# Kernel optimization log

Hardware: AMD Instinct MI355X
Metric: run time of the kernel (lower is better)

The kernel has to match this reference:

```python
import jax, jax.numpy as jnp
import numpy as np

B, S, E, H, L = 4, 1024, 1024, 16, 4
D = E // H
MAX_POS = 1024
NI, NS = 10000, 1000
W_SCALE = 0.02


def setup_inputs() -> dict:
    key = jax.random.key(0)
    ks = jax.random.split(key, 24)
    r = lambda k, sh: jax.random.normal(k, sh, dtype=jnp.float32) * W_SCALE
    return {
        'item_inputs': jax.random.randint(ks[0], (B, S), 0, NI),
        'skill_inputs': jax.random.randint(ks[1], (B, S), 0, NS),
        'label_inputs': jax.random.randint(ks[2], (B, S), 0, 2),
        'item_ids': jax.random.randint(ks[3], (B, S), 0, NI),
        'skill_ids': jax.random.randint(ks[4], (B, S), 0, NS),
        'emb_item': r(ks[5], (NI, E)),
        'emb_skill': r(ks[6], (NS, E)),
        'W_in': r(ks[7], (E, 2 * E)),
        'b_in': r(ks[8], (E,)),
        'Wq': r(ks[9], (L, E, E)),
        'bq': r(ks[10], (L, E)),
        'Wk': r(ks[11], (L, E, E)),
        'bk': r(ks[12], (L, E)),
        'Wv': r(ks[13], (L, E, E)),
        'bv': r(ks[14], (L, E)),
        'Wg': r(ks[15], (L, H, E)),
        'bg': r(ks[16], (L, H)),
        'pos_key': r(ks[17], (L, MAX_POS, D)),
        'Wl': r(ks[18], (L, 3, E, E)),
        'bl': r(ks[19], (L, 3, E)),
        'W_out': r(ks[20], (1, E)),
        'b_out': r(ks[21], (1,)),
    }


def _forward(item_inputs, skill_inputs, emb_item, emb_skill, W_in, b_in,
             Wq, bq, Wk, bk, Wv, bv, Wg, bg, pos_key, Wl, bl, W_out, b_out):
    # input embedding: concat(item, skill) -> linear
    x = jnp.concatenate([emb_item[item_inputs], emb_skill[skill_inputs]], axis=-1)
    x = x @ W_in.T + b_in  # [B, S, E]
    pos_ids = jnp.clip(jnp.arange(S), 0, MAX_POS - 1)
    inv_sqrt_d = 1.0 / np.sqrt(D).astype(np.float32)
    for l in range(L):
        # NOTE (faithful to source): k and v are computed from q0 = linear_q(x)
        q0 = x @ Wq[l].T + bq[l]
        k = q0 @ Wk[l].T + bk[l]
        v = q0 @ Wv[l].T + bv[l]
        # global bias: [B, S, H] -> [B, H, S, 1] (broadcast over key dim)
        glo = jnp.transpose(k @ Wg[l].T + bg[l], (0, 2, 1))[..., None]
        qh = q0.reshape(B, S, H, D).transpose(0, 2, 1, 3)  # [B,H,S,D]
        kh = k.reshape(B, S, H, D).transpose(0, 2, 1, 3)
        vh = v.reshape(B, S, H, D).transpose(0, 2, 1, 3)
        pe = pos_key[l][pos_ids]  # [S, D]
        scores = (jnp.einsum('bhqd,bhkd->bhqk', qh, kh)
                  + glo
                  + jnp.einsum('bhqd,kd->bhqk', qh, pe)) * inv_sqrt_d
        prob = jax.nn.softmax(scores, axis=-1)
        o = jnp.einsum('bhqk,bhkd->bhqd', prob, vh)
        o = o.transpose(0, 2, 1, 3).reshape(B, S, E)
        for i in range(3):  # GELU MLP stack
            o = jax.nn.gelu(o @ Wl[l, i].T + bl[l, i], approximate=False)
        x = o
    out = x @ W_out.T + b_out  # [B, S, 1]
    return out[..., 0]


def reference(item_inputs, skill_inputs, label_inputs, item_ids, skill_ids,
              emb_item, emb_skill, W_in, b_in, Wq, bq, Wk, bk, Wv, bv,
              Wg, bg, pos_key, Wl, bl, W_out, b_out):
    return _forward(item_inputs, skill_inputs, emb_item, emb_skill, W_in, b_in,
                    Wq, bq, Wk, bk, Wv, bv, Wg, bg, pos_key, Wl, bl, W_out, b_out)
```

## Files before the change

kernel.cpp:

```cpp
#include <hip/hip_runtime.h>
#include <hip/hip_bf16.h>


#define B_ 4
#define S_ 1024
#define E_ 1024
#define H_ 16
#define D_ 64
#define L_ 4
#define M_ (B_ * S_)
#define EE (E_ * E_)

typedef __attribute__((ext_vector_type(8))) __bf16 bf16x8;
typedef __attribute__((ext_vector_type(4))) __bf16 bf16x4;
typedef __attribute__((ext_vector_type(4))) float f32x4;
typedef __attribute__((ext_vector_type(8))) unsigned short u16x8;

__device__ __forceinline__ float bf2f(unsigned short u) {
    union { unsigned int i; float f; } x;
    x.i = ((unsigned int)u) << 16;
    return x.f;
}
__device__ __forceinline__ float gelu_exact(float x) {
    return 0.5f * x * (1.0f + erff(x * 0.70710678118654752f));
}

__device__ __forceinline__ size_t kpack_idx(int m, int col) {
    const int b = m >> 10, srow = m & (S_ - 1);
    const int h = col >> 6, d = col & 63;
    const int bh = b * H_ + h;
    const int kt = srow >> 6, kb = (srow >> 4) & 3, l15 = srow & 15;
    const int kc = d >> 5, lhi = (d >> 3) & 3, j = d & 7;
    const int frag = ((bh * 16 + kt) * 4 + kb) * 2 + kc;
    return (size_t)frag * 512 + (size_t)(lhi * 16 + l15) * 8 + j;
}
__device__ __forceinline__ size_t vpack_idx(int m, int col) {
    const int b = m >> 10, key = m & (S_ - 1);
    const int h = col >> 6, d = col & 63;
    const int bh = b * H_ + h;
    const int kt = key >> 6;
    const int k6 = key & 63;
    const int kc = k6 >> 5, kl = k6 & 31;
    const int lhi = (kl >> 2) & 3;
    const int j = ((kl >> 4) << 2) | (kl & 3);
    const int db = d >> 4, l15 = d & 15;
    const int frag = ((bh * 16 + kt) * 4 + db) * 2 + kc;
    return (size_t)frag * 512 + (size_t)(lhi * 16 + l15) * 8 + j;
}

__global__ __launch_bounds__(256) void cvt_f32_bf16(
    const float* __restrict__ in, __bf16* __restrict__ out, int n) {
    const int i = (blockIdx.x * 256 + threadIdx.x) * 4;
    if (i >= n) return;
    const float4 v = *(const float4*)(in + i);
    __bf16* o = out + i;
    o[0] = (__bf16)v.x; o[1] = (__bf16)v.y; o[2] = (__bf16)v.z; o[3] = (__bf16)v.w;
}

__global__ __launch_bounds__(256) void cvt_layer_weights(
    const float* __restrict__ Wq, const float* __restrict__ Wk,
    const float* __restrict__ Wv, const float* __restrict__ Wl,
    __bf16* __restrict__ out) {
    const int i = (blockIdx.x * 256 + threadIdx.x) * 4;
    const int mat = i >> 20;
    const int off = i & (EE - 1);
    const float* src = (mat == 0) ? Wq : (mat == 1) ? Wk : (mat == 2) ? Wv
                                        : Wl + (size_t)(mat - 3) * EE;
    const float4 v = *(const float4*)(src + off);
    __bf16* o = out + i;
    o[0] = (__bf16)v.x; o[1] = (__bf16)v.y; o[2] = (__bf16)v.z; o[3] = (__bf16)v.w;
}

__global__ __launch_bounds__(256) void embed_gather(
    const int* __restrict__ item_idx, const int* __restrict__ skill_idx,
    const float* __restrict__ emb_item, const float* __restrict__ emb_skill,
    __bf16* __restrict__ Xc) {
    const int r = blockIdx.x;
    const int c = threadIdx.x * 8;
    const float* s = (c < E_) ? emb_item + (size_t)item_idx[r] * E_ + c
                              : emb_skill + (size_t)skill_idx[r] * E_ + (c - E_);
    const float4 a = *(const float4*)s;
    const float4 b = *(const float4*)(s + 4);
    __bf16* o = Xc + (size_t)r * 2048 + c;
    o[0] = (__bf16)a.x; o[1] = (__bf16)a.y; o[2] = (__bf16)a.z; o[3] = (__bf16)a.w;
    o[4] = (__bf16)b.x; o[5] = (__bf16)b.y; o[6] = (__bf16)b.z; o[7] = (__bf16)b.w;
}

template <int ACT, int ADD_PE, int PACK>
__global__ __launch_bounds__(256) void gemm_bf16(
    const __bf16* __restrict__ A, const __bf16* __restrict__ Bm,
    const float* __restrict__ bias, __bf16* __restrict__ C, int K,
    const float* __restrict__ pe, const float* __restrict__ bias2) {
    __shared__ __bf16 As[128 * 64];
    __shared__ __bf16 Bs[64 * 64];
    const int tid = threadIdx.x;
    const int lane = tid & 63;
    const int wid = tid >> 6;
    const int wm = wid >> 1;
    const int wn = wid & 1;
    const int l15 = lane & 15, lhi = lane >> 4;

    const int gx = gridDim.x;
    const int id = blockIdx.y * gx + blockIdx.x;
    const int nwg = gx * gridDim.y;
    const int swz = (id & 7) * (nwg >> 3) + (id >> 3);
    const int m0 = (swz / gx) * 128;
    const int n0 = (swz % gx) * 64;

    const __bf16* pa[4];
    __bf16* la[4];
#pragma unroll
    for (int j = 0; j < 4; ++j) {
        const int ca = wid * 256 + j * 64 + lane;
        const int row = ca >> 3, ch = ca & 7;
        pa[j] = A + (size_t)(m0 + row) * K + ((ch ^ (row & 7)) << 3);
        la[j] = As + (size_t)ca * 8;
    }
    const __bf16* pb[2];
    __bf16* lb[2];
#pragma unroll
    for (int j = 0; j < 2; ++j) {
        const int cb = wid * 128 + j * 64 + lane;
        const int row = cb >> 3, ch = cb & 7;
        pb[j] = Bm + (size_t)(n0 + row) * K + ((ch ^ (row & 7)) << 3);
        lb[j] = Bs + (size_t)cb * 8;
    }

    int aoff[4][2], boff[2][2];
#pragma unroll
    for (int mi = 0; mi < 4; ++mi) {
        const int row = wm * 64 + mi * 16 + l15;
#pragma unroll
        for (int kc = 0; kc < 2; ++kc)
            aoff[mi][kc] = row * 64 + (((kc * 4 + lhi) ^ (row & 7)) << 3);
    }
#pragma unroll
    for (int ni = 0; ni < 2; ++ni) {
        const int row = wn * 32 + ni * 16 + l15;
#pragma unroll
        for (int kc = 0; kc < 2; ++kc)
            boff[ni][kc] = row * 64 + (((kc * 4 + lhi) ^ (row & 7)) << 3);
    }

    f32x4 acc[4][2] = {};

    for (int k0 = 0; k0 < K; k0 += 64) {
#pragma unroll
        for (int j = 0; j < 4; ++j)
            __builtin_amdgcn_global_load_lds(
                (const __attribute__((address_space(1))) unsigned int*)(pa[j] + k0),
                (__attribute__((address_space(3))) unsigned int*)la[j], 16, 0, 0);
#pragma unroll
        for (int j = 0; j < 2; ++j)
            __builtin_amdgcn_global_load_lds(
                (const __attribute__((address_space(1))) unsigned int*)(pb[j] + k0),
                (__attribute__((address_space(3))) unsigned int*)lb[j], 16, 0, 0);
        __syncthreads();
        bf16x8 af[4][2], bfr[2][2];
#pragma unroll
        for (int mi = 0; mi < 4; ++mi)
#pragma unroll
            for (int kc = 0; kc < 2; ++kc)
                af[mi][kc] = *(const bf16x8*)(As + aoff[mi][kc]);
#pragma unroll
        for (int ni = 0; ni < 2; ++ni)
#pragma unroll
            for (int kc = 0; kc < 2; ++kc)
                bfr[ni][kc] = *(const bf16x8*)(Bs + boff[ni][kc]);
#pragma unroll
        for (int mi = 0; mi < 4; ++mi)
#pragma unroll
            for (int ni = 0; ni < 2; ++ni)
#pragma unroll
                for (int kc = 0; kc < 2; ++kc)
                    acc[mi][ni] = __builtin_amdgcn_mfma_f32_16x16x32_bf16(
                        af[mi][kc], bfr[ni][kc], acc[mi][ni], 0, 0, 0);
        __syncthreads();
    }

    const int ccol0 = n0 + wn * 32 + l15;
    const int crow0 = m0 + wm * 64 + (lhi << 2);
#pragma unroll
    for (int mi = 0; mi < 4; ++mi) {
#pragma unroll
        for (int ni = 0; ni < 2; ++ni) {
            const int col = ccol0 + ni * 16;
            float bsum;
            if (PACK == 3) bsum = (col < 1024) ? bias[col] : bias2[col - 1024];
            else bsum = bias[col];
#pragma unroll
            for (int r = 0; r < 4; ++r) {
                const int row = crow0 + mi * 16 + r;
                float v = acc[mi][ni][r] + bsum;
                if (ADD_PE) v += pe[((row & (S_ - 1)) << 6) + (col & (D_ - 1))];
                if (ACT) v = gelu_exact(v);
                if (PACK == 0) {
                    C[(size_t)row * E_ + col] = (__bf16)v;
                } else if (PACK == 1) {
                    C[kpack_idx(row, col)] = (__bf16)v;
                } else if (PACK == 2) {
                    C[vpack_idx(row, col)] = (__bf16)v;
                } else {
                    if (col < 1024) {
                        v += pe[((row & (S_ - 1)) << 6) + (col & (D_ - 1))];
                        C[kpack_idx(row, col)] = (__bf16)v;
                    } else {
                        C[(size_t)M_ * E_ + vpack_idx(row, col - 1024)] = (__bf16)v;
                    }
                }
            }
        }
    }
}

__global__ __launch_bounds__(512) void attn_mfma(
    const __bf16* __restrict__ Q, const __bf16* __restrict__ Kp,
    const __bf16* __restrict__ Vp, __bf16* __restrict__ O) {
    __shared__ __bf16 Slds[2][2][8 * 512];
    const int tid = threadIdx.x;
    const int lane = tid & 63;
    const int w = tid >> 6;
    const int l15 = lane & 15, lhi = lane >> 4;

    const int id = blockIdx.y * gridDim.x + blockIdx.x;
    const int swz = (id & 7) * 64 + (id >> 3);
    const int q0 = (swz & 7) * 128 + w * 16;
    const int bh = swz >> 3;
    const int bb = bh >> 4, hh = bh & 15;

    bf16x8 qf[2];
    {
        const __bf16* qrow =
            Q + (size_t)(bb * S_ + q0 + l15) * E_ + hh * 64 + lhi * 8;
#pragma unroll
        for (int kc = 0; kc < 2; ++kc) {
            const u16x8 raw = *(const u16x8*)(qrow + kc * 32);
            bf16x8 v;
#pragma unroll
            for (int j = 0; j < 8; ++j) v[j] = (__bf16)(bf2f(raw[j]) * 0.125f);
            qf[kc] = v;
        }
    }

    const __bf16* kpw = Kp + ((size_t)bh * 16 * 8 + w) * 512 + lane * 8;
    const __bf16* vpw = Vp + ((size_t)bh * 16 * 8 + w) * 512 + lane * 8;

    float m_l = -1e30f, l_l = 0.f;
    f32x4 oacc[4] = {};

    __builtin_amdgcn_global_load_lds(
        (const __attribute__((address_space(1))) unsigned int*)(kpw),
        (__attribute__((address_space(3))) unsigned int*)(&Slds[0][0][w * 512]),
        16, 0, 0);
    __builtin_amdgcn_global_load_lds(
        (const __attribute__((address_space(1))) unsigned int*)(vpw),
        (__attribute__((address_space(3))) unsigned int*)(&Slds[0][1][w * 512]),
        16, 0, 0);

#pragma unroll 2
    for (int kt = 0; kt < S_ / 64; ++kt) {
        const int cur = kt & 1;
        __syncthreads();
        if (kt < S_ / 64 - 1) {
            const size_t fo = (size_t)(kt + 1) * 8 * 512;
            __builtin_amdgcn_global_load_lds(
                (const __attribute__((address_space(1))) unsigned int*)(kpw + fo),
                (__attribute__((address_space(3))) unsigned int*)(
                    &Slds[cur ^ 1][0][w * 512]), 16, 0, 0);
            __builtin_amdgcn_global_load_lds(
                (const __attribute__((address_space(1))) unsigned int*)(vpw + fo),
                (__attribute__((address_space(3))) unsigned int*)(
                    &Slds[cur ^ 1][1][w * 512]), 16, 0, 0);
        }
        const __bf16* kl = &Slds[cur][0][0];
        const __bf16* vl = &Slds[cur][1][0];
        f32x4 s[4];
#pragma unroll
        for (int kb = 0; kb < 4; ++kb) {
            const bf16x8 k0 = *(const bf16x8*)(kl + (kb * 2 + 0) * 512 + lane * 8);
            const bf16x8 k1 = *(const bf16x8*)(kl + (kb * 2 + 1) * 512 + lane * 8);
            f32x4 z = {};
            z = __builtin_amdgcn_mfma_f32_16x16x32_bf16(k0, qf[0], z, 0, 0, 0);
            s[kb] = __builtin_amdgcn_mfma_f32_16x16x32_bf16(k1, qf[1], z, 0, 0, 0);
        }
        float mx0 = fmaxf(fmaxf(s[0][0], s[0][1]), fmaxf(s[0][2], s[0][3]));
        float mx1 = fmaxf(fmaxf(s[1][0], s[1][1]), fmaxf(s[1][2], s[1][3]));
        float mx2 = fmaxf(fmaxf(s[2][0], s[2][1]), fmaxf(s[2][2], s[2][3]));
        float mx3 = fmaxf(fmaxf(s[3][0], s[3][1]), fmaxf(s[3][2], s[3][3]));
        float mx = fmaxf(fmaxf(mx0, mx1), fmaxf(mx2, mx3));
        mx = fmaxf(mx, __shfl_xor(mx, 16));
        mx = fmaxf(mx, __shfl_xor(mx, 32));
        const float mnew = fmaxf(m_l, mx);
        const float corr = __expf(m_l - mnew);
        float p[4][4];
        float rs = 0.f;
#pragma unroll
        for (int kb = 0; kb < 4; ++kb) {
            float sb = 0.f;
#pragma unroll
            for (int r = 0; r < 4; ++r) {
                p[kb][r] = __expf(s[kb][r] - mnew);
                sb += p[kb][r];
            }
            rs += sb;
        }
        rs += __shfl_xor(rs, 16);
        rs += __shfl_xor(rs, 32);
        l_l = l_l * corr + rs;
        m_l = mnew;
#pragma unroll
        for (int db = 0; db < 4; ++db)
#pragma unroll
            for (int r = 0; r < 4; ++r) oacc[db][r] *= corr;
        bf16x8 pf[2];
#pragma unroll
        for (int kc = 0; kc < 2; ++kc) {
            bf16x8 v;
#pragma unroll
            for (int r = 0; r < 4; ++r) {
                v[r] = (__bf16)p[kc * 2][r];
                v[r + 4] = (__bf16)p[kc * 2 + 1][r];
            }
            pf[kc] = v;
        }
#pragma unroll
        for (int db = 0; db < 4; ++db) {
            const bf16x8 v0 = *(const bf16x8*)(vl + (db * 2 + 0) * 512 + lane * 8);
            const bf16x8 v1 = *(const bf16x8*)(vl + (db * 2 + 1) * 512 + lane * 8);
            oacc[db] = __builtin_amdgcn_mfma_f32_16x16x32_bf16(v0, pf[0], oacc[db], 0, 0, 0);
            oacc[db] = __builtin_amdgcn_mfma_f32_16x16x32_bf16(v1, pf[1], oacc[db], 0, 0, 0);
        }
    }
    const float inv_l = 1.f / l_l;
    __bf16* orow = O + (size_t)(bb * S_ + q0 + l15) * E_ + hh * 64 + lhi * 4;
#pragma unroll
    for (int db = 0; db < 4; ++db) {
        bf16x4 ov;
#pragma unroll
        for (int r = 0; r < 4; ++r) ov[r] = (__bf16)(oacc[db][r] * inv_l);
        *(bf16x4*)(orow + db * 16) = ov;
    }
}

__global__ __launch_bounds__(256) void final_proj(
    const __bf16* __restrict__ X, const float* __restrict__ Wout,
    const float* __restrict__ bout, float* __restrict__ out) {
    const int wid = threadIdx.x >> 6, lane = threadIdx.x & 63;
    const int m = blockIdx.x * 4 + wid;
    const __bf16* xrow = X + (size_t)m * E_;
    float acc = 0.f;
#pragma unroll
    for (int c = 0; c < 2; ++c) {
        const int idx = c * 512 + lane * 8;
        const u16x8 xv = *(const u16x8*)(xrow + idx);
        const float4 w1 = *(const float4*)(Wout + idx);
        const float4 w2 = *(const float4*)(Wout + idx + 4);
        acc += bf2f(xv[0]) * w1.x + bf2f(xv[1]) * w1.y + bf2f(xv[2]) * w1.z +
               bf2f(xv[3]) * w1.w + bf2f(xv[4]) * w2.x + bf2f(xv[5]) * w2.y +
               bf2f(xv[6]) * w2.z + bf2f(xv[7]) * w2.w;
    }
#pragma unroll
    for (int off = 32; off; off >>= 1) acc += __shfl_xor(acc, off, 64);
    if (lane == 0) out[m] = acc + bout[0];
}

extern "C" void kernel_launch(void* const* d_in, const int* in_sizes, int n_in,
                              void* d_out, int out_size, void* d_ws, size_t ws_size,
                              hipStream_t stream) {
    const int* item_inputs = (const int*)d_in[0];
    const int* skill_inputs = (const int*)d_in[1];
    const float* emb_item = (const float*)d_in[5];
    const float* emb_skill = (const float*)d_in[6];
    const float* W_in = (const float*)d_in[7];
    const float* b_in = (const float*)d_in[8];
    const float* Wq = (const float*)d_in[9];
    const float* bq = (const float*)d_in[10];
    const float* Wk = (const float*)d_in[11];
    const float* bk = (const float*)d_in[12];
    const float* Wv = (const float*)d_in[13];
    const float* bv = (const float*)d_in[14];
    const float* pos_key = (const float*)d_in[17];
    const float* Wl = (const float*)d_in[18];
    const float* bl = (const float*)d_in[19];
    const float* W_out = (const float*)d_in[20];
    const float* b_out = (const float*)d_in[21];
    float* out = (float*)d_out;

    const size_t SZ = (size_t)M_ * E_;
    __bf16* Xc = (__bf16*)d_ws;
    __bf16* X = Xc + (size_t)M_ * 2048;
    __bf16* Qb = X + SZ;
    __bf16* Kp = Qb + SZ;
    __bf16* Vp = Kp + SZ;
    __bf16* Winb = Vp + SZ;
    __bf16* Wbuf = Winb + 2 * EE;

    const dim3 gg(E_ / 64, M_ / 128);
    const dim3 ggkv(2 * E_ / 64, M_ / 128);
    const dim3 bb(256);

    embed_gather<<<dim3(M_), bb, 0, stream>>>(item_inputs, skill_inputs,
                                              emb_item, emb_skill, Xc);
    cvt_f32_bf16<<<dim3(2 * EE / 1024), bb, 0, stream>>>(W_in, Winb, 2 * EE);
    gemm_bf16<0, 0, 0><<<gg, bb, 0, stream>>>(Xc, Winb, b_in, X, 2048, nullptr, nullptr);

    for (int l = 0; l < L_; ++l) {
        cvt_layer_weights<<<dim3(6 * EE / 1024), bb, 0, stream>>>(
            Wq + (size_t)l * EE, Wk + (size_t)l * EE, Wv + (size_t)l * EE,
            Wl + (size_t)l * 3 * EE, Wbuf);
        const float* pe_l = pos_key + (size_t)l * S_ * D_;
        gemm_bf16<0, 0, 0><<<gg, bb, 0, stream>>>(X, Wbuf + 0 * EE, bq + l * E_, Qb, E_, nullptr, nullptr);
        gemm_bf16<0, 0, 3><<<ggkv, bb, 0, stream>>>(Qb, Wbuf + 1 * EE, bk + l * E_, Kp, E_, pe_l, bv + l * E_);
        attn_mfma<<<dim3(S_ / 128, B_ * H_), dim3(512), 0, stream>>>(Qb, Kp, Vp, X);
        gemm_bf16<1, 0, 0><<<gg, bb, 0, stream>>>(X, Wbuf + 3 * EE, bl + (l * 3 + 0) * E_, Qb, E_, nullptr, nullptr);
        gemm_bf16<1, 0, 0><<<gg, bb, 0, stream>>>(Qb, Wbuf + 4 * EE, bl + (l * 3 + 1) * E_, Kp, E_, nullptr, nullptr);
        gemm_bf16<1, 0, 0><<<gg, bb, 0, stream>>>(Kp, Wbuf + 5 * EE, bl + (l * 3 + 2) * E_, X, E_, nullptr, nullptr);
    }
    final_proj<<<dim3(M_ / 4), bb, 0, stream>>>(X, W_out, b_out, out);
}
```

Baseline: 598.5 us.

## Double-buffer GEMM LDS tiles and convert all layer weights in one launch

The GEMM now uses two LDS buffers per operand and issues the async global-to-LDS loads for the next K tile before computing on the current one. This overlaps memory latency with MFMA work and needs one barrier per iteration instead of two. The per-layer weight conversion kernels are merged into a single up-front launch that writes all layers into one larger workspace, removing three launches. The cost is doubled LDS per block, which may reduce occupancy, and a larger workspace requirement.

```diff
diff --git a/kernel.cpp b/kernel.cpp
--- a/kernel.cpp
+++ b/kernel.cpp
@@ -57,15 +57,19 @@
     o[0] = (__bf16)v.x; o[1] = (__bf16)v.y; o[2] = (__bf16)v.z; o[3] = (__bf16)v.w;
 }
 
-__global__ __launch_bounds__(256) void cvt_layer_weights(
+__global__ __launch_bounds__(256) void cvt_all_weights(
     const float* __restrict__ Wq, const float* __restrict__ Wk,
     const float* __restrict__ Wv, const float* __restrict__ Wl,
     __bf16* __restrict__ out) {
     const int i = (blockIdx.x * 256 + threadIdx.x) * 4;
-    const int mat = i >> 20;
-    const int off = i & (EE - 1);
-    const float* src = (mat == 0) ? Wq : (mat == 1) ? Wk : (mat == 2) ? Wv
-                                        : Wl + (size_t)(mat - 3) * EE;
+    const int l = i / (6 * EE);
+    const int r = i - l * 6 * EE;
+    const int mat = r >> 20;
+    const int off = r & (EE - 1);
+    const float* src = (mat == 0) ? Wq + (size_t)l * EE
+                     : (mat == 1) ? Wk + (size_t)l * EE
+                     : (mat == 2) ? Wv + (size_t)l * EE
+                                  : Wl + ((size_t)l * 3 + (mat - 3)) * EE;
     const float4 v = *(const float4*)(src + off);
     __bf16* o = out + i;
     o[0] = (__bf16)v.x; o[1] = (__bf16)v.y; o[2] = (__bf16)v.z; o[3] = (__bf16)v.w;
@@ -91,8 +95,8 @@
     const __bf16* __restrict__ A, const __bf16* __restrict__ Bm,
     const float* __restrict__ bias, __bf16* __restrict__ C, int K,
     const float* __restrict__ pe, const float* __restrict__ bias2) {
-    __shared__ __bf16 As[128 * 64];
-    __shared__ __bf16 Bs[64 * 64];
+    __shared__ __bf16 As[2][128 * 64];
+    __shared__ __bf16 Bs[2][64 * 64];
     const int tid = threadIdx.x;
     const int lane = tid & 63;
     const int wid = tid >> 6;
@@ -108,22 +112,22 @@
     const int n0 = (swz % gx) * 64;
 
     const __bf16* pa[4];
-    __bf16* la[4];
+    int laoff[4];
 #pragma unroll
     for (int j = 0; j < 4; ++j) {
         const int ca = wid * 256 + j * 64 + lane;
         const int row = ca >> 3, ch = ca & 7;
         pa[j] = A + (size_t)(m0 + row) * K + ((ch ^ (row & 7)) << 3);
-        la[j] = As + (size_t)ca * 8;
+        laoff[j] = ca * 8;
     }
     const __bf16* pb[2];
-    __bf16* lb[2];
+    int lboff[2];
 #pragma unroll
     for (int j = 0; j < 2; ++j) {
         const int cb = wid * 128 + j * 64 + lane;
         const int row = cb >> 3, ch = cb & 7;
         pb[j] = Bm + (size_t)(n0 + row) * K + ((ch ^ (row & 7)) << 3);
-        lb[j] = Bs + (size_t)cb * 8;
+        lboff[j] = cb * 8;
     }
 
     int aoff[4][2], boff[2][2];
@@ -143,30 +147,50 @@
     }
 
     f32x4 acc[4][2] = {};
-
-    for (int k0 = 0; k0 < K; k0 += 64) {
-#pragma unroll
-        for (int j = 0; j < 4; ++j)
-            __builtin_amdgcn_global_load_lds(
-                (const __attribute__((address_space(1))) unsigned int*)(pa[j] + k0),
-                (__attribute__((address_space(3))) unsigned int*)la[j], 16, 0, 0);
-#pragma unroll
-        for (int j = 0; j < 2; ++j)
-            __builtin_amdgcn_global_load_lds(
-                (const __attribute__((address_space(1))) unsigned int*)(pb[j] + k0),
-                (__attribute__((address_space(3))) unsigned int*)lb[j], 16, 0, 0);
+    const int NT = K >> 6;
+
+#pragma unroll
+    for (int j = 0; j < 4; ++j)
+        __builtin_amdgcn_global_load_lds(
+            (const __attribute__((address_space(1))) unsigned int*)(pa[j]),
+            (__attribute__((address_space(3))) unsigned int*)(&As[0][0] + laoff[j]),
+            16, 0, 0);
+#pragma unroll
+    for (int j = 0; j < 2; ++j)
+        __builtin_amdgcn_global_load_lds(
+            (const __attribute__((address_space(1))) unsigned int*)(pb[j]),
+            (__attribute__((address_space(3))) unsigned int*)(&Bs[0][0] + lboff[j]),
+            16, 0, 0);
+
+    for (int t = 0; t < NT; ++t) {
+        const int cur = t & 1;
         __syncthreads();
+        if (t + 1 < NT) {
+            const size_t koff = (size_t)(t + 1) << 6;
+#pragma unroll
+            for (int j = 0; j < 4; ++j)
+                __builtin_amdgcn_global_load_lds(
+                    (const __attribute__((address_space(1))) unsigned int*)(pa[j] + koff),
+                    (__attribute__((address_space(3))) unsigned int*)(
+                        &As[cur ^ 1][0] + laoff[j]), 16, 0, 0);
+#pragma unroll
+            for (int j = 0; j < 2; ++j)
+                __builtin_amdgcn_global_load_lds(
+                    (const __attribute__((address_space(1))) unsigned int*)(pb[j] + koff),
+                    (__attribute__((address_space(3))) unsigned int*)(
+                        &Bs[cur ^ 1][0] + lboff[j]), 16, 0, 0);
+        }
         bf16x8 af[4][2], bfr[2][2];
 #pragma unroll
         for (int mi = 0; mi < 4; ++mi)
 #pragma unroll
             for (int kc = 0; kc < 2; ++kc)
-                af[mi][kc] = *(const bf16x8*)(As + aoff[mi][kc]);
+                af[mi][kc] = *(const bf16x8*)(&As[cur][0] + aoff[mi][kc]);
 #pragma unroll
         for (int ni = 0; ni < 2; ++ni)
 #pragma unroll
             for (int kc = 0; kc < 2; ++kc)
-                bfr[ni][kc] = *(const bf16x8*)(Bs + boff[ni][kc]);
+                bfr[ni][kc] = *(const bf16x8*)(&Bs[cur][0] + boff[ni][kc]);
 #pragma unroll
         for (int mi = 0; mi < 4; ++mi)
 #pragma unroll
@@ -175,7 +199,6 @@
                 for (int kc = 0; kc < 2; ++kc)
                     acc[mi][ni] = __builtin_amdgcn_mfma_f32_16x16x32_bf16(
                         af[mi][kc], bfr[ni][kc], acc[mi][ni], 0, 0, 0);
-        __syncthreads();
     }
 
     const int ccol0 = n0 + wn * 32 + l15;
@@ -393,7 +416,7 @@
     __bf16* Kp = Qb + SZ;
     __bf16* Vp = Kp + SZ;
     __bf16* Winb = Vp + SZ;
-    __bf16* Wbuf = Winb + 2 * EE;
+    __bf16* Wall = Winb + 2 * EE;
 
     const dim3 gg(E_ / 64, M_ / 128);
     const dim3 ggkv(2 * E_ / 64, M_ / 128);
@@ -402,12 +425,11 @@
     embed_gather<<<dim3(M_), bb, 0, stream>>>(item_inputs, skill_inputs,
                                               emb_item, emb_skill, Xc);
     cvt_f32_bf16<<<dim3(2 * EE / 1024), bb, 0, stream>>>(W_in, Winb, 2 * EE);
+    cvt_all_weights<<<dim3(L_ * 6 * EE / 1024), bb, 0, stream>>>(Wq, Wk, Wv, Wl, Wall);
     gemm_bf16<0, 0, 0><<<gg, bb, 0, stream>>>(Xc, Winb, b_in, X, 2048, nullptr, nullptr);
 
     for (int l = 0; l < L_; ++l) {
-        cvt_layer_weights<<<dim3(6 * EE / 1024), bb, 0, stream>>>(
-            Wq + (size_t)l * EE, Wk + (size_t)l * EE, Wv + (size_t)l * EE,
-            Wl + (size_t)l * 3 * EE, Wbuf);
+        __bf16* Wbuf = Wall + (size_t)l * 6 * EE;
         const float* pe_l = pos_key + (size_t)l * S_ * D_;
         gemm_bf16<0, 0, 0><<<gg, bb, 0, stream>>>(X, Wbuf + 0 * EE, bq + l * E_, Qb, E_, nullptr, nullptr);
         gemm_bf16<0, 0, 3><<<ggkv, bb, 0, stream>>>(Qb, Wbuf + 1 * EE, bk + l * E_, Kp, E_, pe_l, bv + l * E_);
```

Result: no change. 596.4 us (-0.4%).

## Split-K the square GEMMs with fp32 partials and convert all weights once

Applied to the files above, without the earlier changes.

The N=1024 GEMMs (input projection, Q, and the three MLP layers) now use a 2-way split-K kernel. Each half writes fp32 partial tiles to a workspace buffer, and a separate epilogue kernel sums the halves and adds bias plus optional GELU. This doubles the workgroup count (512 to 1024 blocks) to fill more CUs. Weight conversion for all layers is also hoisted into a single launch before the layer loop. The split-K path adds substantial extra global traffic (two 16 MB fp32 partials written and read per GEMM) and an extra launch per GEMM.

```diff
diff --git a/kernel.cpp b/kernel.cpp
--- a/kernel.cpp
+++ b/kernel.cpp
@@ -57,15 +57,19 @@
     o[0] = (__bf16)v.x; o[1] = (__bf16)v.y; o[2] = (__bf16)v.z; o[3] = (__bf16)v.w;
 }
 
-__global__ __launch_bounds__(256) void cvt_layer_weights(
+__global__ __launch_bounds__(256) void cvt_all_weights(
     const float* __restrict__ Wq, const float* __restrict__ Wk,
     const float* __restrict__ Wv, const float* __restrict__ Wl,
     __bf16* __restrict__ out) {
     const int i = (blockIdx.x * 256 + threadIdx.x) * 4;
-    const int mat = i >> 20;
-    const int off = i & (EE - 1);
-    const float* src = (mat == 0) ? Wq : (mat == 1) ? Wk : (mat == 2) ? Wv
-                                        : Wl + (size_t)(mat - 3) * EE;
+    const int l = i / (6 * EE);
+    const int r = i - l * 6 * EE;
+    const int mat = r >> 20;
+    const int off = r & (EE - 1);
+    const float* src = (mat == 0) ? Wq + (size_t)l * EE
+                     : (mat == 1) ? Wk + (size_t)l * EE
+                     : (mat == 2) ? Wv + (size_t)l * EE
+                                  : Wl + ((size_t)l * 3 + (mat - 3)) * EE;
     const float4 v = *(const float4*)(src + off);
     __bf16* o = out + i;
     o[0] = (__bf16)v.x; o[1] = (__bf16)v.y; o[2] = (__bf16)v.z; o[3] = (__bf16)v.w;
@@ -86,8 +90,138 @@
     o[4] = (__bf16)b.x; o[5] = (__bf16)b.y; o[6] = (__bf16)b.z; o[7] = (__bf16)b.w;
 }
 
-template <int ACT, int ADD_PE, int PACK>
-__global__ __launch_bounds__(256) void gemm_bf16(
+__global__ __launch_bounds__(256) void gemm_ks(
+    const __bf16* __restrict__ A, const __bf16* __restrict__ Bm,
+    float* __restrict__ P, int K) {
+    __shared__ __bf16 As[128 * 64];
+    __shared__ __bf16 Bs[64 * 64];
+    const int tid = threadIdx.x;
+    const int lane = tid & 63;
+    const int wid = tid >> 6;
+    const int wm = wid >> 1;
+    const int wn = wid & 1;
+    const int l15 = lane & 15, lhi = lane >> 4;
+
+    const int gx = gridDim.x;
+    const int per_z = gx * gridDim.y;
+    const int id = (blockIdx.z * gridDim.y + blockIdx.y) * gx + blockIdx.x;
+    const int nwg = per_z * 2;
+    const int swz = (id & 7) * (nwg >> 3) + (id >> 3);
+    const int z2 = swz / per_z;
+    const int rem = swz - z2 * per_z;
+    const int m0 = (rem / gx) * 128;
+    const int n0 = (rem - (rem / gx) * gx) * 64;
+    const int kbase = z2 * (K >> 1);
+
+    const __bf16* pa[4];
+    __bf16* la[4];
+#pragma unroll
+    for (int j = 0; j < 4; ++j) {
+        const int ca = wid * 256 + j * 64 + lane;
+        const int row = ca >> 3, ch = ca & 7;
+        pa[j] = A + (size_t)(m0 + row) * K + ((ch ^ (row & 7)) << 3) + kbase;
+        la[j] = As + (size_t)ca * 8;
+    }
+    const __bf16* pb[2];
+    __bf16* lb[2];
+#pragma unroll
+    for (int j = 0; j < 2; ++j) {
+        const int cb = wid * 128 + j * 64 + lane;
+        const int row = cb >> 3, ch = cb & 7;
+        pb[j] = Bm + (size_t)(n0 + row) * K + ((ch ^ (row & 7)) << 3) + kbase;
+        lb[j] = Bs + (size_t)cb * 8;
+    }
+
+    int aoff[4][2], boff[2][2];
+#pragma unroll
+    for (int mi = 0; mi < 4; ++mi) {
+        const int row = wm * 64 + mi * 16 + l15;
+#pragma unroll
+        for (int kc = 0; kc < 2; ++kc)
+            aoff[mi][kc] = row * 64 + (((kc * 4 + lhi) ^ (row & 7)) << 3);
+    }
+#pragma unroll
+    for (int ni = 0; ni < 2; ++ni) {
+        const int row = wn * 32 + ni * 16 + l15;
+#pragma unroll
+        for (int kc = 0; kc < 2; ++kc)
+            boff[ni][kc] = row * 64 + (((kc * 4 + lhi) ^ (row & 7)) << 3);
+    }
+
+    f32x4 acc[4][2] = {};
+    const int KH = K >> 1;
+
+    for (int k0 = 0; k0 < KH; k0 += 64) {
+#pragma unroll
+        for (int j = 0; j < 4; ++j)
+            __builtin_amdgcn_global_load_lds(
+                (const __attribute__((address_space(1))) unsigned int*)(pa[j] + k0),
+                (__attribute__((address_space(3))) unsigned int*)la[j], 16, 0, 0);
+#pragma unroll
+        for (int j = 0; j < 2; ++j)
+            __builtin_amdgcn_global_load_lds(
+                (const __attribute__((address_space(1))) unsigned int*)(pb[j] + k0),
+                (__attribute__((address_space(3))) unsigned int*)lb[j], 16, 0, 0);
+        __syncthreads();
+        bf16x8 af[4][2], bfr[2][2];
+#pragma unroll
+        for (int mi = 0; mi < 4; ++mi)
+#pragma unroll
+            for (int kc = 0; kc < 2; ++kc)
+                af[mi][kc] = *(const bf16x8*)(As + aoff[mi][kc]);
+#pragma unroll
+        for (int ni = 0; ni < 2; ++ni)
+#pragma unroll
+            for (int kc = 0; kc < 2; ++kc)
+                bfr[ni][kc] = *(const bf16x8*)(Bs + boff[ni][kc]);
+#pragma unroll
+        for (int mi = 0; mi < 4; ++mi)
+#pragma unroll
+            for (int ni = 0; ni < 2; ++ni)
+#pragma unroll
+                for (int kc = 0; kc < 2; ++kc)
+                    acc[mi][ni] = __builtin_amdgcn_mfma_f32_16x16x32_bf16(
+                        af[mi][kc], bfr[ni][kc], acc[mi][ni], 0, 0, 0);
+        __syncthreads();
+    }
+
+    float* Pz = P + (size_t)z2 * M_ * E_;
+    const int ccol0 = n0 + wn * 32 + l15;
+    const int crow0 = m0 + wm * 64 + (lhi << 2);
+#pragma unroll
+    for (int mi = 0; mi < 4; ++mi)
+#pragma unroll
+        for (int ni = 0; ni < 2; ++ni) {
+            const int col = ccol0 + ni * 16;
+#pragma unroll
+            for (int r = 0; r < 4; ++r)
+                Pz[(size_t)(crow0 + mi * 16 + r) * E_ + col] = acc[mi][ni][r];
+        }
+}
+
+template <int ACT>
+__global__ __launch_bounds__(256) void ep_sum(
+    const float* __restrict__ P, const float* __restrict__ bias,
+    __bf16* __restrict__ C) {
+    const size_t idx = ((size_t)blockIdx.x * 256 + threadIdx.x) * 8;
+    const int col = (int)(idx & (E_ - 1));
+    const float4 a0 = *(const float4*)(P + idx);
+    const float4 a1 = *(const float4*)(P + idx + 4);
+    const float4 b0 = *(const float4*)(P + (size_t)M_ * E_ + idx);
+    const float4 b1 = *(const float4*)(P + (size_t)M_ * E_ + idx + 4);
+    const float4 s0 = *(const float4*)(bias + col);
+    const float4 s1 = *(const float4*)(bias + col + 4);
+    float v[8] = {a0.x + b0.x + s0.x, a0.y + b0.y + s0.y,
+                  a0.z + b0.z + s0.z, a0.w + b0.w + s0.w,
+                  a1.x + b1.x + s1.x, a1.y + b1.y + s1.y,
+                  a1.z + b1.z + s1.z, a1.w + b1.w + s1.w};
+    bf16x8 o;
+#pragma unroll
+    for (int j = 0; j < 8; ++j) o[j] = (__bf16)(ACT ? gelu_exact(v[j]) : v[j]);
+    *(bf16x8*)(C + idx) = o;
+}
+
+__global__ __launch_bounds__(256) void gemm_kv(
     const __bf16* __restrict__ A, const __bf16* __restrict__ Bm,
     const float* __restrict__ bias, __bf16* __restrict__ C, int K,
     const float* __restrict__ pe, const float* __restrict__ bias2) {
@@ -185,28 +319,16 @@
 #pragma unroll
         for (int ni = 0; ni < 2; ++ni) {
             const int col = ccol0 + ni * 16;
-            float bsum;
-            if (PACK == 3) bsum = (col < 1024) ? bias[col] : bias2[col - 1024];
-            else bsum = bias[col];
+            const float bsum = (col < 1024) ? bias[col] : bias2[col - 1024];
 #pragma unroll
             for (int r = 0; r < 4; ++r) {
                 const int row = crow0 + mi * 16 + r;
                 float v = acc[mi][ni][r] + bsum;
-                if (ADD_PE) v += pe[((row & (S_ - 1)) << 6) + (col & (D_ - 1))];
-                if (ACT) v = gelu_exact(v);
-                if (PACK == 0) {
-                    C[(size_t)row * E_ + col] = (__bf16)v;
-                } else if (PACK == 1) {
+                if (col < 1024) {
+                    v += pe[((row & (S_ - 1)) << 6) + (col & (D_ - 1))];
                     C[kpack_idx(row, col)] = (__bf16)v;
-                } else if (PACK == 2) {
-                    C[vpack_idx(row, col)] = (__bf16)v;
                 } else {
-                    if (col < 1024) {
-                        v += pe[((row & (S_ - 1)) << 6) + (col & (D_ - 1))];
-                        C[kpack_idx(row, col)] = (__bf16)v;
-                    } else {
-                        C[(size_t)M_ * E_ + vpack_idx(row, col - 1024)] = (__bf16)v;
-                    }
+                    C[(size_t)M_ * E_ + vpack_idx(row, col - 1024)] = (__bf16)v;
                 }
             }
         }
@@ -393,28 +515,36 @@
     __bf16* Kp = Qb + SZ;
     __bf16* Vp = Kp + SZ;
     __bf16* Winb = Vp + SZ;
-    __bf16* Wbuf = Winb + 2 * EE;
-
-    const dim3 gg(E_ / 64, M_ / 128);
-    const dim3 ggkv(2 * E_ / 64, M_ / 128);
+    __bf16* Wall = Winb + 2 * EE;
+    float* Pbuf = (float*)(Wall + (size_t)L_ * 6 * EE);
+
+    const dim3 ggks(16, 32, 2);
+    const dim3 ggkv(32, 32);
+    const dim3 gge(2048);
     const dim3 bb(256);
 
     embed_gather<<<dim3(M_), bb, 0, stream>>>(item_inputs, skill_inputs,
                                               emb_item, emb_skill, Xc);
     cvt_f32_bf16<<<dim3(2 * EE / 1024), bb, 0, stream>>>(W_in, Winb, 2 * EE);
-    gemm_bf16<0, 0, 0><<<gg, bb, 0, stream>>>(Xc, Winb, b_in, X, 2048, nullptr, nullptr);
+    cvt_all_weights<<<dim3(L_ * 6 * EE / 1024), bb, 0, stream>>>(Wq, Wk, Wv, Wl, Wall);
+
+    gemm_ks<<<ggks, bb, 0, stream>>>(Xc, Winb, Pbuf, 2048);
+    ep_sum<0><<<gge, bb, 0, stream>>>(Pbuf, b_in, X);
 
     for (int l = 0; l < L_; ++l) {
-        cvt_layer_weights<<<dim3(6 * EE / 1024), bb, 0, stream>>>(
-            Wq + (size_t)l * EE, Wk + (size_t)l * EE, Wv + (size_t)l * EE,
-            Wl + (size_t)l * 3 * EE, Wbuf);
+        __bf16* Wbuf = Wall + (size_t)l * 6 * EE;
         const float* pe_l = pos_key + (size_t)l * S_ * D_;
-        gemm_bf16<0, 0, 0><<<gg, bb, 0, stream>>>(X, Wbuf + 0 * EE, bq + l * E_, Qb, E_, nullptr, nullptr);
-        gemm_bf16<0, 0, 3><<<ggkv, bb, 0, stream>>>(Qb, Wbuf + 1 * EE, bk + l * E_, Kp, E_, pe_l, bv + l * E_);
+        gemm_ks<<<ggks, bb, 0, stream>>>(X, Wbuf + 0 * EE, Pbuf, E_);
+        ep_sum<0><<<gge, bb, 0, stream>>>(Pbuf, bq + l * E_, Qb);
+        gemm_kv<<<ggkv, bb, 0, stream>>>(Qb, Wbuf + 1 * EE, bk + l * E_, Kp, E_,
+                                         pe_l, bv + l * E_);
         attn_mfma<<<dim3(S_ / 128, B_ * H_), dim3(512), 0, stream>>>(Qb, Kp, Vp, X);
-        gemm_bf16<1, 0, 0><<<gg, bb, 0, stream>>>(X, Wbuf + 3 * EE, bl + (l * 3 + 0) * E_, Qb, E_, nullptr, nullptr);
-        gemm_bf16<1, 0, 0><<<gg, bb, 0, stream>>>(Qb, Wbuf + 4 * EE, bl + (l * 3 + 1) * E_, Kp, E_, nullptr, nullptr);
-        gemm_bf16<1, 0, 0><<<gg, bb, 0, stream>>>(Kp, Wbuf + 5 * EE, bl + (l * 3 + 2) * E_, X, E_, nullptr, nullptr);
+        gemm_ks<<<ggks, bb, 0, stream>>>(X, Wbuf + 3 * EE, Pbuf, E_);
+        ep_sum<1><<<gge, bb, 0, stream>>>(Pbuf, bl + (l * 3 + 0) * E_, Qb);
+        gemm_ks<<<ggks, bb, 0, stream>>>(Qb, Wbuf + 4 * EE, Pbuf, E_);
+        ep_sum<1><<<gge, bb, 0, stream>>>(Pbuf, bl + (l * 3 + 1) * E_, Kp);
+        gemm_ks<<<ggks, bb, 0, stream>>>(Kp, Wbuf + 5 * EE, Pbuf, E_);
+        ep_sum<1><<<gge, bb, 0, stream>>>(Pbuf, bl + (l * 3 + 2) * E_, X);
     }
     final_proj<<<dim3(M_ / 4), bb, 0, stream>>>(X, W_out, b_out, out);
 }
```

Result: slower. 694.2 us (+16.0%).
